# Kernel tuning notes

Measured on AMD Instinct MI355X. Metric: run time of the kernel, lower is better.

The kernel has to match this reference:

```python
import jax, jax.numpy as jnp
import numpy as np

D, K, H1, H2 = 768, 4, 512, 256
B = 16384

def layer_norm(x, g, b, eps=1e-5):
    mu = jnp.mean(x, axis=-1, keepdims=True)
    xc = x - mu
    var = jnp.mean(xc * xc, axis=-1, keepdims=True)
    return xc * jax.lax.rsqrt(var + eps) * g + b

def setup_inputs() -> dict:
    key = jax.random.key(0)
    ks = jax.random.split(key, 8)
    def lin(k, fan_in, fan_out):
        bound = 1.0 / np.sqrt(fan_in)
        kw, kb = jax.random.split(k)
        W = jax.random.uniform(kw, (fan_in, fan_out), jnp.float32, -bound, bound)
        b = jax.random.uniform(kb, (fan_out,), jnp.float32, -bound, bound)
        return W, b
    W1, b1 = lin(ks[0], D, H1)
    W2, b2 = lin(ks[1], H1, H2)
    Wd, bd = lin(ks[2], H2, K * D)
    Wa, ba = lin(ks[3], H2, D)
    return {
        "embeddings": jax.random.normal(ks[4], (B, D), jnp.float32),
        "W1": W1, "b1": b1, "g1": jnp.ones((H1,), jnp.float32), "be1": jnp.zeros((H1,), jnp.float32),
        "W2": W2, "b2": b2, "g2": jnp.ones((H2,), jnp.float32), "be2": jnp.zeros((H2,), jnp.float32),
        "Wd": Wd, "bd": bd, "Wa": Wa, "ba": ba,
    }

def _forward(embeddings, W1, b1, g1, be1, W2, b2, g2, be2, Wd, bd, Wa, ba):
    h = jax.nn.relu(layer_norm(embeddings @ W1 + b1, g1, be1))  # (B, H1)
    h = jax.nn.relu(layer_norm(h @ W2 + b2, g2, be2))           # (B, H2)
    W_flat = h @ Wd + bd                                         # (B, K*D)
    W = W_flat.reshape(-1, K, D)
    attn = jax.nn.softmax(h @ Wa + ba, axis=-1)                  # (B, D)
    W = W * attn[:, None, :]
    # sequential Gram-Schmidt over k (small fixed K, unrolled)
    ortho = []
    for i in range(K):
        v = W[:, i, :]
        for u in ortho:
            proj = jnp.sum(v * u, axis=-1, keepdims=True)
            v = v - proj * u
        norm = jnp.maximum(jnp.linalg.norm(v, axis=-1, keepdims=True), 1e-12)
        ortho.append(v / norm)
    W_ortho = jnp.stack(ortho, axis=1)  # (B, K, D)
    return W_ortho, attn

def reference(embeddings, W1, b1, g1, be1, W2, b2, g2, be2, Wd, bd, Wa, ba):
    return _forward(embeddings, W1, b1, g1, be1, W2, b2, g2, be2, Wd, bd, Wa, ba)
```

## Files before the change

### kernel.cpp

```cpp
#include <hip/hip_runtime.h>
#include <hip/hip_bf16.h>

#define BSZ 16384
#define DD  768
#define KK  4
#define NH1 512
#define NH2 256
#define ND  (KK * DD)

typedef __bf16 bf16x8 __attribute__((ext_vector_type(8)));
typedef float  f32x4  __attribute__((ext_vector_type(4)));

static __device__ __forceinline__ float bf2f(ushort u) {
    union { unsigned int i; float f; } v; v.i = (unsigned int)u << 16; return v.f;
}
static __device__ __forceinline__ ushort f2bf(float f) {
    return __bfloat16_as_ushort(__float2bfloat16(f));
}
static __device__ __forceinline__ void gload_lds16(const void* g, void* l) {
    __builtin_amdgcn_global_load_lds(
        (const __attribute__((address_space(1))) void*)g,
        (__attribute__((address_space(3))) void*)l, 16, 0, 0);
}

__global__ __launch_bounds__(256) void k_cvt_emb(
    const float* __restrict__ src, ushort* __restrict__ dst, int n8)
{
    const int stride = gridDim.x * 256;
    for (int i = blockIdx.x * 256 + threadIdx.x; i < n8; i += stride) {
        float4 a = *(const float4*)&src[(size_t)i * 8];
        float4 b = *(const float4*)&src[(size_t)i * 8 + 4];
        ushort u[8];
        u[0] = f2bf(a.x); u[1] = f2bf(a.y); u[2] = f2bf(a.z); u[3] = f2bf(a.w);
        u[4] = f2bf(b.x); u[5] = f2bf(b.y); u[6] = f2bf(b.z); u[7] = f2bf(b.w);
        *(int4*)&dst[(size_t)i * 8] = *(int4*)u;
    }
}

__global__ __launch_bounds__(256) void k_t_cvt(
    const float* __restrict__ src, ushort* __restrict__ dst, int R, int C)
{
    __shared__ float tile[32][33];
    const int rb0 = blockIdx.y * 32;
    const int cb0 = blockIdx.x * 32;
    const int t = threadIdx.x;
    const int r = t >> 5, c = t & 31;
    #pragma unroll
    for (int i = 0; i < 4; ++i)
        tile[r + i * 8][c] = src[(size_t)(rb0 + r + i * 8) * C + cb0 + c];
    __syncthreads();
    #pragma unroll
    for (int i = 0; i < 4; ++i)
        dst[(size_t)(cb0 + r + i * 8) * R + rb0 + c] = f2bf(tile[c][r + i * 8]);
}

__global__ __launch_bounds__(256) void k1_gemm(
    const ushort* __restrict__ embb, const ushort* __restrict__ W1t,
    const float* __restrict__ b1, ushort* __restrict__ h1raw)
{
    __shared__ ushort smem[2 * 128 * 64];
    ushort* Asm = smem;
    ushort* Bsm = smem + 128 * 64;

    const int t    = threadIdx.x;
    const int lane = t & 63;
    const int wid  = t >> 6;
    const int wm   = wid >> 1;
    const int wn   = wid & 1;
    const int l16  = lane & 15;
    const int sl0  = lane >> 4;
    const int g4   = (lane >> 4) * 4;

    const int srow = lane >> 3;
    const int ssl  = (lane & 7) ^ srow;

    const int rb = blockIdx.y * 128;
    const int cb = blockIdx.x * 128;

    f32x4 acc[4][4] = {};

    for (int ks = 0; ks < 12; ++ks) {
        const int k0 = ks * 64;
        __syncthreads();
        #pragma unroll
        for (int i = 0; i < 4; ++i) {
            const int stripe = wid * 4 + i;
            const int row    = stripe * 8 + srow;
            gload_lds16(&embb[(size_t)(rb + row) * DD + k0 + ssl * 8],
                        &Asm[stripe * 512]);
            gload_lds16(&W1t [(size_t)(cb + row) * DD + k0 + ssl * 8],
                        &Bsm[stripe * 512]);
        }
        __syncthreads();

        #pragma unroll
        for (int kk = 0; kk < 2; ++kk) {
            const int slot = kk * 4 + sl0;
            bf16x8 af[4], bfr[4];
            #pragma unroll
            for (int m = 0; m < 4; ++m) {
                const int R = wm * 64 + m * 16 + l16;
                af[m] = *(const bf16x8*)&Asm[R * 64 + (slot ^ (R & 7)) * 8];
            }
            #pragma unroll
            for (int n = 0; n < 4; ++n) {
                const int R = wn * 64 + n * 16 + l16;
                bfr[n] = *(const bf16x8*)&Bsm[R * 64 + (slot ^ (R & 7)) * 8];
            }
            #pragma unroll
            for (int m = 0; m < 4; ++m)
                #pragma unroll
                for (int n = 0; n < 4; ++n)
                    acc[m][n] = __builtin_amdgcn_mfma_f32_16x16x32_bf16(
                        af[m], bfr[n], acc[m][n], 0, 0, 0);
        }
    }

    float bv[4];
    #pragma unroll
    for (int n = 0; n < 4; ++n)
        bv[n] = b1[cb + wn * 64 + n * 16 + l16];

    __syncthreads();
    #pragma unroll
    for (int m = 0; m < 4; ++m)
        #pragma unroll
        for (int n = 0; n < 4; ++n)
            #pragma unroll
            for (int j = 0; j < 4; ++j)
                smem[(wm * 64 + m * 16 + g4 + j) * 128 + wn * 64 + n * 16 + l16] =
                    f2bf(acc[m][n][j] + bv[n]);
    __syncthreads();
    #pragma unroll
    for (int i = 0; i < 8; ++i) {
        int ch  = t + i * 256;
        int row = ch >> 4;
        int q   = ch & 15;
        *(int4*)&h1raw[(size_t)(rb + row) * NH1 + cb + q * 8] =
            *(const int4*)&smem[row * 128 + q * 8];
    }
}

__global__ __launch_bounds__(256) void k1_ln(
    ushort* h1, const float* __restrict__ g1, const float* __restrict__ be1)
{
    const int lane = threadIdx.x & 63;
    const int w    = threadIdx.x >> 6;
    const size_t row = (size_t)blockIdx.x * 4 + w;

    ushort* p = h1 + row * NH1 + lane * 8;
    ushort u[8];
    *(int4*)u = *(const int4*)p;
    float x[8];
    float s = 0.f, q = 0.f;
    #pragma unroll
    for (int j = 0; j < 8; ++j) {
        x[j] = bf2f(u[j]);
        s += x[j];
        q += x[j] * x[j];
    }
    #pragma unroll
    for (int off = 32; off; off >>= 1) {
        s += __shfl_xor(s, off);
        q += __shfl_xor(q, off);
    }
    const float mu  = s * (1.f / NH1);
    const float var = q * (1.f / NH1) - mu * mu;
    const float rs  = rsqrtf(var + 1e-5f);

    float gv[8], ev[8];
    *(float4*)&gv[0] = *(const float4*)&g1[lane * 8];
    *(float4*)&gv[4] = *(const float4*)&g1[lane * 8 + 4];
    *(float4*)&ev[0] = *(const float4*)&be1[lane * 8];
    *(float4*)&ev[4] = *(const float4*)&be1[lane * 8 + 4];
    #pragma unroll
    for (int j = 0; j < 8; ++j)
        u[j] = f2bf(fmaxf(fmaf((x[j] - mu) * rs, gv[j], ev[j]), 0.f));
    *(int4*)p = *(int4*)u;
}

__global__ __launch_bounds__(512) void k2_mfma(
    const ushort* __restrict__ h1, const ushort* __restrict__ W2t,
    const float* __restrict__ b2, const float* __restrict__ g2,
    const float* __restrict__ be2, ushort* __restrict__ h2)
{
    __shared__ ushort Asm[64 * 64];
    __shared__ ushort Bsm[256 * 64];
    __shared__ float red[8][64][2];
    __shared__ float stats[64][2];

    const int t    = threadIdx.x;
    const int lane = t & 63;
    const int wid  = t >> 6;
    const int wm   = wid >> 2;
    const int wn   = wid & 3;
    const int l16  = lane & 15;
    const int sl0  = lane >> 4;
    const int g4   = (lane >> 4) * 4;
    const int rb   = blockIdx.x * 64;

    const int srow = lane >> 3;
    const int ssl  = (lane & 7) ^ srow;

    f32x4 acc[2][4] = {};

    for (int ks = 0; ks < 8; ++ks) {
        const int k0 = ks * 64;
        __syncthreads();
        {
            const int row = wid * 8 + srow;
            gload_lds16(&h1[(size_t)(rb + row) * NH1 + k0 + ssl * 8],
                        &Asm[wid * 512]);
        }
        #pragma unroll
        for (int i = 0; i < 4; ++i) {
            const int stripe = wid * 4 + i;
            const int row    = stripe * 8 + srow;
            gload_lds16(&W2t[(size_t)row * NH1 + k0 + ssl * 8],
                        &Bsm[stripe * 512]);
        }
        __syncthreads();

        #pragma unroll
        for (int kk = 0; kk < 2; ++kk) {
            const int slot = kk * 4 + sl0;
            bf16x8 af[2], bfr[4];
            #pragma unroll
            for (int m = 0; m < 2; ++m) {
                const int R = wm * 32 + m * 16 + l16;
                af[m] = *(const bf16x8*)&Asm[R * 64 + (slot ^ (R & 7)) * 8];
            }
            #pragma unroll
            for (int n = 0; n < 4; ++n) {
                const int R = wn * 64 + n * 16 + l16;
                bfr[n] = *(const bf16x8*)&Bsm[R * 64 + (slot ^ (R & 7)) * 8];
            }
            #pragma unroll
            for (int m = 0; m < 2; ++m)
                #pragma unroll
                for (int n = 0; n < 4; ++n)
                    acc[m][n] = __builtin_amdgcn_mfma_f32_16x16x32_bf16(
                        af[m], bfr[n], acc[m][n], 0, 0, 0);
        }
    }

    float bv[4];
    #pragma unroll
    for (int n = 0; n < 4; ++n) bv[n] = b2[wn * 64 + n * 16 + l16];
    #pragma unroll
    for (int m = 0; m < 2; ++m)
        #pragma unroll
        for (int n = 0; n < 4; ++n)
            #pragma unroll
            for (int j = 0; j < 4; ++j) acc[m][n][j] += bv[n];

    #pragma unroll
    for (int m = 0; m < 2; ++m)
        #pragma unroll
        for (int j = 0; j < 4; ++j) {
            float p = 0.f, q = 0.f;
            #pragma unroll
            for (int n = 0; n < 4; ++n) {
                float v = acc[m][n][j];
                p += v; q += v * v;
            }
            #pragma unroll
            for (int off = 8; off; off >>= 1) {
                p += __shfl_xor(p, off);
                q += __shfl_xor(q, off);
            }
            if (l16 == 0) {
                red[wid][wm * 32 + m * 16 + g4 + j][0] = p;
                red[wid][wm * 32 + m * 16 + g4 + j][1] = q;
            }
        }
    __syncthreads();
    if (t < 64) {
        const int w0 = (t >> 5) * 4;
        float S = 0.f, S2 = 0.f;
        #pragma unroll
        for (int w = 0; w < 4; ++w) { S += red[w0 + w][t][0]; S2 += red[w0 + w][t][1]; }
        float mu  = S  * (1.f / NH2);
        float var = S2 * (1.f / NH2) - mu * mu;
        stats[t][0] = mu;
        stats[t][1] = rsqrtf(var + 1e-5f);
    }
    __syncthreads();

    float gv[4], ev[4];
    #pragma unroll
    for (int n = 0; n < 4; ++n) {
        int col = wn * 64 + n * 16 + l16;
        gv[n] = g2[col]; ev[n] = be2[col];
    }
    ushort* dst = h2 + (size_t)rb * NH2;
    #pragma unroll
    for (int m = 0; m < 2; ++m)
        #pragma unroll
        for (int j = 0; j < 4; ++j) {
            int row = wm * 32 + m * 16 + g4 + j;
            float mu = stats[row][0], rs = stats[row][1];
            #pragma unroll
            for (int n = 0; n < 4; ++n) {
                float val = fmaxf(fmaf((acc[m][n][j] - mu) * rs, gv[n], ev[n]), 0.f);
                dst[(size_t)row * NH2 + wn * 64 + n * 16 + l16] = f2bf(val);
            }
        }
}

__global__ __launch_bounds__(256) void k_gemm_wd_mfma(
    const ushort* __restrict__ h2, const ushort* __restrict__ Wdt,
    const float* __restrict__ bd, ushort* __restrict__ outw)
{
    __shared__ ushort smem[2 * 128 * 64];
    ushort* Asm = smem;
    ushort* Bsm = smem + 128 * 64;

    const int t    = threadIdx.x;
    const int lane = t & 63;
    const int wid  = t >> 6;
    const int wm   = wid >> 1;
    const int wn   = wid & 1;
    const int l16  = lane & 15;
    const int sl0  = lane >> 4;
    const int g4   = (lane >> 4) * 4;

    const int srow = lane >> 3;
    const int ssl  = (lane & 7) ^ srow;

    const int rb = blockIdx.y * 128;
    const int cb = blockIdx.x * 128;

    f32x4 acc[4][4] = {};

    for (int ks = 0; ks < 4; ++ks) {
        const int k0 = ks * 64;
        __syncthreads();
        #pragma unroll
        for (int i = 0; i < 4; ++i) {
            const int stripe = wid * 4 + i;
            const int row    = stripe * 8 + srow;
            gload_lds16(&h2 [(size_t)(rb + row) * NH2 + k0 + ssl * 8],
                        &Asm[stripe * 512]);
            gload_lds16(&Wdt[(size_t)(cb + row) * NH2 + k0 + ssl * 8],
                        &Bsm[stripe * 512]);
        }
        __syncthreads();

        #pragma unroll
        for (int kk = 0; kk < 2; ++kk) {
            const int slot = kk * 4 + sl0;
            bf16x8 af[4], bfr[4];
            #pragma unroll
            for (int m = 0; m < 4; ++m) {
                const int R = wm * 64 + m * 16 + l16;
                af[m] = *(const bf16x8*)&Asm[R * 64 + (slot ^ (R & 7)) * 8];
            }
            #pragma unroll
            for (int n = 0; n < 4; ++n) {
                const int R = wn * 64 + n * 16 + l16;
                bfr[n] = *(const bf16x8*)&Bsm[R * 64 + (slot ^ (R & 7)) * 8];
            }
            #pragma unroll
            for (int m = 0; m < 4; ++m)
                #pragma unroll
                for (int n = 0; n < 4; ++n)
                    acc[m][n] = __builtin_amdgcn_mfma_f32_16x16x32_bf16(
                        af[m], bfr[n], acc[m][n], 0, 0, 0);
        }
    }

    float bv[4];
    #pragma unroll
    for (int n = 0; n < 4; ++n)
        bv[n] = bd[cb + wn * 64 + n * 16 + l16];

    __syncthreads();
    #pragma unroll
    for (int m = 0; m < 4; ++m)
        #pragma unroll
        for (int n = 0; n < 4; ++n)
            #pragma unroll
            for (int j = 0; j < 4; ++j)
                smem[(wm * 64 + m * 16 + g4 + j) * 128 + wn * 64 + n * 16 + l16] =
                    f2bf(acc[m][n][j] + bv[n]);
    __syncthreads();
    #pragma unroll
    for (int i = 0; i < 8; ++i) {
        int ch  = t + i * 256;
        int row = ch >> 4;
        int q   = ch & 15;
        *(int4*)&outw[(size_t)(rb + row) * 6144 + 3072 + cb + q * 8] =
            *(const int4*)&smem[row * 128 + q * 8];
    }
}

__global__ __launch_bounds__(512) void k_attn_gs_mfma(
    const ushort* __restrict__ h2, const ushort* __restrict__ Wat,
    const float* __restrict__ ba, float* __restrict__ out)
{
    __shared__ ushort Asm[64 * 64];
    __shared__ ushort Bsm[768 * 64];
    __shared__ float red[8][64];
    __shared__ float stats[64];

    const int t    = threadIdx.x;
    const int lane = t & 63;
    const int wid  = t >> 6;
    const int wm   = wid >> 2;
    const int wn   = wid & 3;
    const int l16  = lane & 15;
    const int sl0  = lane >> 4;
    const int g4   = (lane >> 4) * 4;
    const int rb   = blockIdx.x * 64;

    const int srow = lane >> 3;
    const int ssl  = (lane & 7) ^ srow;

    float* attn = out + (size_t)BSZ * (KK * DD);

    f32x4 acc[2][12] = {};

    for (int ks = 0; ks < 4; ++ks) {
        const int k0 = ks * 64;
        __syncthreads();
        {
            const int row = wid * 8 + srow;
            gload_lds16(&h2[(size_t)(rb + row) * NH2 + k0 + ssl * 8],
                        &Asm[wid * 512]);
        }
        #pragma unroll
        for (int i = 0; i < 12; ++i) {
            const int stripe = wid * 12 + i;
            const int row    = stripe * 8 + srow;
            gload_lds16(&Wat[(size_t)row * NH2 + k0 + ssl * 8],
                        &Bsm[stripe * 512]);
        }
        __syncthreads();

        #pragma unroll
        for (int kk = 0; kk < 2; ++kk) {
            const int slot = kk * 4 + sl0;
            bf16x8 af[2], bfr[12];
            #pragma unroll
            for (int m = 0; m < 2; ++m) {
                const int R = wm * 32 + m * 16 + l16;
                af[m] = *(const bf16x8*)&Asm[R * 64 + (slot ^ (R & 7)) * 8];
            }
            #pragma unroll
            for (int n = 0; n < 12; ++n) {
                const int R = wn * 192 + n * 16 + l16;
                bfr[n] = *(const bf16x8*)&Bsm[R * 64 + (slot ^ (R & 7)) * 8];
            }
            #pragma unroll
            for (int m = 0; m < 2; ++m)
                #pragma unroll
                for (int n = 0; n < 12; ++n)
                    acc[m][n] = __builtin_amdgcn_mfma_f32_16x16x32_bf16(
                        af[m], bfr[n], acc[m][n], 0, 0, 0);
        }
    }

    float bb[12];
    #pragma unroll
    for (int n = 0; n < 12; ++n) bb[n] = ba[wn * 192 + n * 16 + l16];
    #pragma unroll
    for (int m = 0; m < 2; ++m)
        #pragma unroll
        for (int n = 0; n < 12; ++n)
            #pragma unroll
            for (int j = 0; j < 4; ++j) acc[m][n][j] += bb[n];

    #pragma unroll
    for (int m = 0; m < 2; ++m)
        #pragma unroll
        for (int j = 0; j < 4; ++j) {
            float p = acc[m][0][j];
            #pragma unroll
            for (int n = 1; n < 12; ++n) p = fmaxf(p, acc[m][n][j]);
            #pragma unroll
            for (int off = 8; off; off >>= 1) p = fmaxf(p, __shfl_xor(p, off));
            if (l16 == 0) red[wid][wm * 32 + m * 16 + g4 + j] = p;
        }
    __syncthreads();
    if (t < 64) {
        const int w0 = (t >> 5) * 4;
        stats[t] = fmaxf(fmaxf(red[w0][t], red[w0 + 1][t]),
                         fmaxf(red[w0 + 2][t], red[w0 + 3][t]));
    }
    __syncthreads();
    #pragma unroll
    for (int m = 0; m < 2; ++m)
        #pragma unroll
        for (int j = 0; j < 4; ++j) {
            float M = stats[wm * 32 + m * 16 + g4 + j];
            float s = 0.f;
            #pragma unroll
            for (int n = 0; n < 12; ++n) {
                acc[m][n][j] = __expf(acc[m][n][j] - M);
                s += acc[m][n][j];
            }
            #pragma unroll
            for (int off = 8; off; off >>= 1) s += __shfl_xor(s, off);
            if (l16 == 0) red[wid][wm * 32 + m * 16 + g4 + j] = s;
        }
    __syncthreads();
    if (t < 64) {
        const int w0 = (t >> 5) * 4;
        stats[t] = 1.f / (red[w0][t] + red[w0 + 1][t] + red[w0 + 2][t] + red[w0 + 3][t]);
    }
    __syncthreads();

    float* stage = (float*)Bsm;
    #pragma unroll
    for (int h = 0; h < 2; ++h) {
        if (wm == h) {
            #pragma unroll
            for (int m = 0; m < 2; ++m)
                #pragma unroll
                for (int j = 0; j < 4; ++j) {
                    const int r = m * 16 + g4 + j;
                    const float inv = stats[h * 32 + r];
                    #pragma unroll
                    for (int n = 0; n < 12; ++n)
                        stage[r * 768 + wn * 192 + n * 16 + l16] = acc[m][n][j] * inv;
                }
        }
        __syncthreads();
        #pragma unroll
        for (int i = 0; i < 12; ++i) {
            int ch  = t + i * 512;
            int row = ch / 192;
            int q   = ch - row * 192;
            *(float4*)&attn[(size_t)(rb + h * 32 + row) * DD + q * 4] =
                *(const float4*)&stage[row * 768 + q * 4];
        }
        for (int rr = 0; rr < 4; ++rr) {
            const int rl = wid * 4 + rr;
            const size_t row = (size_t)rb + h * 32 + rl;
            float a[12];
            #pragma unroll
            for (int k = 0; k < 3; ++k)
                *(float4*)&a[k * 4] =
                    *(const float4*)&stage[rl * 768 + lane * 4 + 256 * k];

            const ushort* wsrc = (const ushort*)out + row * 6144 + 3072;
            float* Wf = out + row * (KK * DD);
            float w[4][12];
            #pragma unroll
            for (int i = 0; i < 4; ++i) {
                #pragma unroll
                for (int k = 0; k < 3; ++k) {
                    ushort4 uv = *(const ushort4*)&wsrc[i * DD + lane * 4 + 256 * k];
                    w[i][k * 4 + 0] = bf2f(uv.x) * a[k * 4 + 0];
                    w[i][k * 4 + 1] = bf2f(uv.y) * a[k * 4 + 1];
                    w[i][k * 4 + 2] = bf2f(uv.z) * a[k * 4 + 2];
                    w[i][k * 4 + 3] = bf2f(uv.w) * a[k * 4 + 3];
                }
            }
            #pragma unroll
            for (int i = 0; i < 4; ++i) {
                #pragma unroll
                for (int p = 0; p < i; ++p) {
                    float s2 = 0.f;
                    #pragma unroll
                    for (int j = 0; j < 12; ++j) s2 = fmaf(w[i][j], w[p][j], s2);
                    #pragma unroll
                    for (int off = 32; off; off >>= 1) s2 += __shfl_xor(s2, off);
                    #pragma unroll
                    for (int j = 0; j < 12; ++j) w[i][j] = fmaf(-s2, w[p][j], w[i][j]);
                }
                float n2 = 0.f;
                #pragma unroll
                for (int j = 0; j < 12; ++j) n2 = fmaf(w[i][j], w[i][j], n2);
                #pragma unroll
                for (int off = 32; off; off >>= 1) n2 += __shfl_xor(n2, off);
                float invn = 1.f / fmaxf(sqrtf(n2), 1e-12f);
                #pragma unroll
                for (int j = 0; j < 12; ++j) w[i][j] *= invn;
            }
            #pragma unroll
            for (int i = 0; i < 4; ++i) {
                #pragma unroll
                for (int k = 0; k < 3; ++k) {
                    float4 wv;
                    wv.x = w[i][k * 4 + 0]; wv.y = w[i][k * 4 + 1];
                    wv.z = w[i][k * 4 + 2]; wv.w = w[i][k * 4 + 3];
                    *(float4*)&Wf[i * DD + lane * 4 + 256 * k] = wv;
                }
            }
        }
        __syncthreads();
    }
}

extern "C" void kernel_launch(void* const* d_in, const int* in_sizes, int n_in,
                              void* d_out, int out_size, void* d_ws, size_t ws_size,
                              hipStream_t stream)
{
    const float* emb = (const float*)d_in[0];
    const float* W1  = (const float*)d_in[1];
    const float* b1  = (const float*)d_in[2];
    const float* g1  = (const float*)d_in[3];
    const float* be1 = (const float*)d_in[4];
    const float* W2  = (const float*)d_in[5];
    const float* b2  = (const float*)d_in[6];
    const float* g2  = (const float*)d_in[7];
    const float* be2 = (const float*)d_in[8];
    const float* Wd  = (const float*)d_in[9];
    const float* bd  = (const float*)d_in[10];
    const float* Wa  = (const float*)d_in[11];
    const float* ba  = (const float*)d_in[12];

    float* out = (float*)d_out;
    ushort* h1   = (ushort*)d_ws;
    ushort* h2   = h1 + (size_t)BSZ * NH1;
    ushort* Wdt  = h2 + (size_t)BSZ * NH2;
    ushort* W1t  = Wdt + (size_t)ND * NH2;
    ushort* W2t  = W1t + (size_t)NH1 * DD;
    ushort* Wat  = W2t + (size_t)NH2 * NH1;
    ushort* embb = Wat + (size_t)DD * NH2;

    hipLaunchKernelGGL(k_cvt_emb, dim3(2048), dim3(256), 0, stream,
                       emb, embb, BSZ * DD / 8);
    hipLaunchKernelGGL(k_t_cvt, dim3(NH1 / 32, DD / 32), dim3(256), 0, stream,
                       W1, W1t, DD, NH1);
    hipLaunchKernelGGL(k_t_cvt, dim3(NH2 / 32, NH1 / 32), dim3(256), 0, stream,
                       W2, W2t, NH1, NH2);
    hipLaunchKernelGGL(k_t_cvt, dim3(ND / 32, NH2 / 32), dim3(256), 0, stream,
                       Wd, Wdt, NH2, ND);
    hipLaunchKernelGGL(k_t_cvt, dim3(DD / 32, NH2 / 32), dim3(256), 0, stream,
                       Wa, Wat, NH2, DD);
    hipLaunchKernelGGL(k1_gemm, dim3(NH1 / 128, BSZ / 128), dim3(256), 0, stream,
                       embb, W1t, b1, h1);
    hipLaunchKernelGGL(k1_ln, dim3(BSZ / 4), dim3(256), 0, stream,
                       h1, g1, be1);
    hipLaunchKernelGGL(k2_mfma, dim3(BSZ / 64), dim3(512), 0, stream,
                       h1, W2t, b2, g2, be2, h2);
    hipLaunchKernelGGL(k_gemm_wd_mfma, dim3(ND / 128, BSZ / 128), dim3(256), 0, stream,
                       h2, Wdt, bd, (ushort*)out);
    hipLaunchKernelGGL(k_attn_gs_mfma, dim3(BSZ / 64), dim3(512), 0, stream,
                       h2, Wat, ba, out);
}
```

Measured before the change: 181.5 us.

## Fuse LN1 into second GEMM and merge prep kernels into one launch

```diff
diff --git a/kernel.cpp b/kernel.cpp
--- a/kernel.cpp
+++ b/kernel.cpp
@@ -23,27 +23,41 @@
         (__attribute__((address_space(3))) void*)l, 16, 0, 0);
 }
 
-__global__ __launch_bounds__(256) void k_cvt_emb(
-    const float* __restrict__ src, ushort* __restrict__ dst, int n8)
-{
-    const int stride = gridDim.x * 256;
-    for (int i = blockIdx.x * 256 + threadIdx.x; i < n8; i += stride) {
-        float4 a = *(const float4*)&src[(size_t)i * 8];
-        float4 b = *(const float4*)&src[(size_t)i * 8 + 4];
-        ushort u[8];
-        u[0] = f2bf(a.x); u[1] = f2bf(a.y); u[2] = f2bf(a.z); u[3] = f2bf(a.w);
-        u[4] = f2bf(b.x); u[5] = f2bf(b.y); u[6] = f2bf(b.z); u[7] = f2bf(b.w);
-        *(int4*)&dst[(size_t)i * 8] = *(int4*)u;
-    }
-}
-
-__global__ __launch_bounds__(256) void k_t_cvt(
-    const float* __restrict__ src, ushort* __restrict__ dst, int R, int C)
+__global__ __launch_bounds__(256) void k_prep(
+    const float* __restrict__ emb, ushort* __restrict__ embb,
+    const float* __restrict__ W1, ushort* __restrict__ W1t,
+    const float* __restrict__ W2, ushort* __restrict__ W2t,
+    const float* __restrict__ Wd, ushort* __restrict__ Wdt,
+    const float* __restrict__ Wa, ushort* __restrict__ Wat)
 {
     __shared__ float tile[32][33];
-    const int rb0 = blockIdx.y * 32;
-    const int cb0 = blockIdx.x * 32;
+    const int bid = blockIdx.x;
     const int t = threadIdx.x;
+
+    if (bid < 2048) {
+        const int n8 = BSZ * DD / 8;
+        const int stride = 2048 * 256;
+        for (int i = bid * 256 + t; i < n8; i += stride) {
+            float4 a = *(const float4*)&emb[(size_t)i * 8];
+            float4 b = *(const float4*)&emb[(size_t)i * 8 + 4];
+            ushort u[8];
+            u[0] = f2bf(a.x); u[1] = f2bf(a.y); u[2] = f2bf(a.z); u[3] = f2bf(a.w);
+            u[4] = f2bf(b.x); u[5] = f2bf(b.y); u[6] = f2bf(b.z); u[7] = f2bf(b.w);
+            *(int4*)&embb[(size_t)i * 8] = *(int4*)u;
+        }
+        return;
+    }
+
+    const float* src; ushort* dst; int R, C, rb0, cb0;
+    if (bid < 2432)      { int l = bid - 2048; src = W1; dst = W1t; R = DD;  C = NH1;
+                           cb0 = (l & 15) * 32; rb0 = (l >> 4) * 32; }
+    else if (bid < 2560) { int l = bid - 2432; src = W2; dst = W2t; R = NH1; C = NH2;
+                           cb0 = (l & 7) * 32;  rb0 = (l >> 3) * 32; }
+    else if (bid < 3328) { int l = bid - 2560; src = Wd; dst = Wdt; R = NH2; C = ND;
+                           cb0 = (l % 96) * 32; rb0 = (l / 96) * 32; }
+    else                 { int l = bid - 3328; src = Wa; dst = Wat; R = NH2; C = DD;
+                           cb0 = (l % 24) * 32; rb0 = (l / 24) * 32; }
+
     const int r = t >> 5, c = t & 31;
     #pragma unroll
     for (int i = 0; i < 4; ++i)
@@ -141,116 +155,129 @@
     }
 }
 
-__global__ __launch_bounds__(256) void k1_ln(
-    ushort* h1, const float* __restrict__ g1, const float* __restrict__ be1)
-{
-    const int lane = threadIdx.x & 63;
-    const int w    = threadIdx.x >> 6;
-    const size_t row = (size_t)blockIdx.x * 4 + w;
-
-    ushort* p = h1 + row * NH1 + lane * 8;
-    ushort u[8];
-    *(int4*)u = *(const int4*)p;
-    float x[8];
-    float s = 0.f, q = 0.f;
-    #pragma unroll
-    for (int j = 0; j < 8; ++j) {
-        x[j] = bf2f(u[j]);
-        s += x[j];
-        q += x[j] * x[j];
-    }
-    #pragma unroll
-    for (int off = 32; off; off >>= 1) {
-        s += __shfl_xor(s, off);
-        q += __shfl_xor(q, off);
-    }
-    const float mu  = s * (1.f / NH1);
-    const float var = q * (1.f / NH1) - mu * mu;
-    const float rs  = rsqrtf(var + 1e-5f);
-
-    float gv[8], ev[8];
-    *(float4*)&gv[0] = *(const float4*)&g1[lane * 8];
-    *(float4*)&gv[4] = *(const float4*)&g1[lane * 8 + 4];
-    *(float4*)&ev[0] = *(const float4*)&be1[lane * 8];
-    *(float4*)&ev[4] = *(const float4*)&be1[lane * 8 + 4];
-    #pragma unroll
-    for (int j = 0; j < 8; ++j)
-        u[j] = f2bf(fmaxf(fmaf((x[j] - mu) * rs, gv[j], ev[j]), 0.f));
-    *(int4*)p = *(int4*)u;
-}
-
 __global__ __launch_bounds__(512) void k2_mfma(
-    const ushort* __restrict__ h1, const ushort* __restrict__ W2t,
+    const ushort* __restrict__ h1raw, const ushort* __restrict__ W2t,
+    const float* __restrict__ g1, const float* __restrict__ be1,
     const float* __restrict__ b2, const float* __restrict__ g2,
     const float* __restrict__ be2, ushort* __restrict__ h2)
 {
-    __shared__ ushort Asm[64 * 64];
+    __shared__ ushort Ah[8 * 2048];
     __shared__ ushort Bsm[256 * 64];
-    __shared__ float red[8][64][2];
-    __shared__ float stats[64][2];
+    __shared__ float red[8][32][2];
+    __shared__ float stats[32][2];
 
     const int t    = threadIdx.x;
     const int lane = t & 63;
     const int wid  = t >> 6;
-    const int wm   = wid >> 2;
-    const int wn   = wid & 3;
     const int l16  = lane & 15;
     const int sl0  = lane >> 4;
     const int g4   = (lane >> 4) * 4;
-    const int rb   = blockIdx.x * 64;
+    const int rb   = blockIdx.x * 32;
 
     const int srow = lane >> 3;
     const int ssl  = (lane & 7) ^ srow;
 
-    f32x4 acc[2][4] = {};
+    #pragma unroll
+    for (int i = 0; i < 4; ++i) {
+        const int s  = wid * 4 + i;
+        const int ks = s >> 2;
+        const int st = s & 3;
+        const int row = st * 8 + srow;
+        gload_lds16(&h1raw[(size_t)(rb + row) * NH1 + ks * 64 + ssl * 8],
+                    &Ah[ks * 2048 + st * 512]);
+    }
+    __syncthreads();
+
+    {
+        const int r  = t >> 4;
+        const int j  = t & 15;
+        const int ks = j >> 1;
+        const int hf = j & 1;
+        ushort u[4][8];
+        float s = 0.f, q2 = 0.f;
+        #pragma unroll
+        for (int qi = 0; qi < 4; ++qi) {
+            const int q = hf * 4 + qi;
+            *(int4*)u[qi] = *(const int4*)
+                &Ah[ks * 2048 + (r >> 3) * 512 + (r & 7) * 64 + ((q ^ (r & 7)) * 8)];
+            #pragma unroll
+            for (int e = 0; e < 8; ++e) {
+                float x = bf2f(u[qi][e]);
+                s += x; q2 += x * x;
+            }
+        }
+        #pragma unroll
+        for (int off = 8; off; off >>= 1) {
+            s  += __shfl_xor(s, off);
+            q2 += __shfl_xor(q2, off);
+        }
+        const float mu  = s * (1.f / NH1);
+        const float var = q2 * (1.f / NH1) - mu * mu;
+        const float rs  = rsqrtf(var + 1e-5f);
+        #pragma unroll
+        for (int qi = 0; qi < 4; ++qi) {
+            const int q = hf * 4 + qi;
+            const int col = ks * 64 + q * 8;
+            float gv[8], ev[8];
+            *(float4*)&gv[0] = *(const float4*)&g1[col];
+            *(float4*)&gv[4] = *(const float4*)&g1[col + 4];
+            *(float4*)&ev[0] = *(const float4*)&be1[col];
+            *(float4*)&ev[4] = *(const float4*)&be1[col + 4];
+            #pragma unroll
+            for (int e = 0; e < 8; ++e) {
+                float x = bf2f(u[qi][e]);
+                u[qi][e] = f2bf(fmaxf(fmaf((x - mu) * rs, gv[e], ev[e]), 0.f));
+            }
+            *(int4*)&Ah[ks * 2048 + (r >> 3) * 512 + (r & 7) * 64 + ((q ^ (r & 7)) * 8)]
+                = *(int4*)u[qi];
+        }
+    }
+
+    f32x4 acc[2][2] = {};
 
     for (int ks = 0; ks < 8; ++ks) {
         const int k0 = ks * 64;
         __syncthreads();
-        {
-            const int row = wid * 8 + srow;
-            gload_lds16(&h1[(size_t)(rb + row) * NH1 + k0 + ssl * 8],
-                        &Asm[wid * 512]);
-        }
         #pragma unroll
         for (int i = 0; i < 4; ++i) {
-            const int stripe = wid * 4 + i;
-            const int row    = stripe * 8 + srow;
+            const int s   = wid * 4 + i;
+            const int row = s * 8 + srow;
             gload_lds16(&W2t[(size_t)row * NH1 + k0 + ssl * 8],
-                        &Bsm[stripe * 512]);
+                        &Bsm[s * 512]);
         }
         __syncthreads();
 
         #pragma unroll
         for (int kk = 0; kk < 2; ++kk) {
             const int slot = kk * 4 + sl0;
-            bf16x8 af[2], bfr[4];
+            bf16x8 af[2], bfr[2];
             #pragma unroll
             for (int m = 0; m < 2; ++m) {
-                const int R = wm * 32 + m * 16 + l16;
-                af[m] = *(const bf16x8*)&Asm[R * 64 + (slot ^ (R & 7)) * 8];
-            }
-            #pragma unroll
-            for (int n = 0; n < 4; ++n) {
-                const int R = wn * 64 + n * 16 + l16;
+                const int R = m * 16 + l16;
+                af[m] = *(const bf16x8*)
+                    &Ah[ks * 2048 + R * 64 + (slot ^ (R & 7)) * 8];
+            }
+            #pragma unroll
+            for (int n = 0; n < 2; ++n) {
+                const int R = wid * 32 + n * 16 + l16;
                 bfr[n] = *(const bf16x8*)&Bsm[R * 64 + (slot ^ (R & 7)) * 8];
             }
             #pragma unroll
             for (int m = 0; m < 2; ++m)
                 #pragma unroll
-                for (int n = 0; n < 4; ++n)
+                for (int n = 0; n < 2; ++n)
                     acc[m][n] = __builtin_amdgcn_mfma_f32_16x16x32_bf16(
                         af[m], bfr[n], acc[m][n], 0, 0, 0);
         }
     }
 
-    float bv[4];
-    #pragma unroll
-    for (int n = 0; n < 4; ++n) bv[n] = b2[wn * 64 + n * 16 + l16];
+    float bv[2];
+    #pragma unroll
+    for (int n = 0; n < 2; ++n) bv[n] = b2[wid * 32 + n * 16 + l16];
     #pragma unroll
     for (int m = 0; m < 2; ++m)
         #pragma unroll
-        for (int n = 0; n < 4; ++n)
+        for (int n = 0; n < 2; ++n)
             #pragma unroll
             for (int j = 0; j < 4; ++j) acc[m][n][j] += bv[n];
 
@@ -260,7 +287,7 @@
         for (int j = 0; j < 4; ++j) {
             float p = 0.f, q = 0.f;
             #pragma unroll
-            for (int n = 0; n < 4; ++n) {
+            for (int n = 0; n < 2; ++n) {
                 float v = acc[m][n][j];
                 p += v; q += v * v;
             }
@@ -270,16 +297,15 @@
                 q += __shfl_xor(q, off);
             }
             if (l16 == 0) {
-                red[wid][wm * 32 + m * 16 + g4 + j][0] = p;
-                red[wid][wm * 32 + m * 16 + g4 + j][1] = q;
-            }
-        }
-    __syncthreads();
-    if (t < 64) {
-        const int w0 = (t >> 5) * 4;
+                red[wid][m * 16 + g4 + j][0] = p;
+                red[wid][m * 16 + g4 + j][1] = q;
+            }
+        }
+    __syncthreads();
+    if (t < 32) {
         float S = 0.f, S2 = 0.f;
         #pragma unroll
-        for (int w = 0; w < 4; ++w) { S += red[w0 + w][t][0]; S2 += red[w0 + w][t][1]; }
+        for (int w = 0; w < 8; ++w) { S += red[w][t][0]; S2 += red[w][t][1]; }
         float mu  = S  * (1.f / NH2);
         float var = S2 * (1.f / NH2) - mu * mu;
         stats[t][0] = mu;
@@ -287,10 +313,10 @@
     }
     __syncthreads();
 
-    float gv[4], ev[4];
-    #pragma unroll
-    for (int n = 0; n < 4; ++n) {
-        int col = wn * 64 + n * 16 + l16;
+    float gv[2], ev[2];
+    #pragma unroll
+    for (int n = 0; n < 2; ++n) {
+        int col = wid * 32 + n * 16 + l16;
         gv[n] = g2[col]; ev[n] = be2[col];
     }
     ushort* dst = h2 + (size_t)rb * NH2;
@@ -298,12 +324,12 @@
     for (int m = 0; m < 2; ++m)
         #pragma unroll
         for (int j = 0; j < 4; ++j) {
-            int row = wm * 32 + m * 16 + g4 + j;
+            int row = m * 16 + g4 + j;
             float mu = stats[row][0], rs = stats[row][1];
             #pragma unroll
-            for (int n = 0; n < 4; ++n) {
+            for (int n = 0; n < 2; ++n) {
                 float val = fmaxf(fmaf((acc[m][n][j] - mu) * rs, gv[n], ev[n]), 0.f);
-                dst[(size_t)row * NH2 + wn * 64 + n * 16 + l16] = f2bf(val);
+                dst[(size_t)row * NH2 + wid * 32 + n * 16 + l16] = f2bf(val);
             }
         }
 }
@@ -621,22 +647,12 @@
     ushort* Wat  = W2t + (size_t)NH2 * NH1;
     ushort* embb = Wat + (size_t)DD * NH2;
 
-    hipLaunchKernelGGL(k_cvt_emb, dim3(2048), dim3(256), 0, stream,
-                       emb, embb, BSZ * DD / 8);
-    hipLaunchKernelGGL(k_t_cvt, dim3(NH1 / 32, DD / 32), dim3(256), 0, stream,
-                       W1, W1t, DD, NH1);
-    hipLaunchKernelGGL(k_t_cvt, dim3(NH2 / 32, NH1 / 32), dim3(256), 0, stream,
-                       W2, W2t, NH1, NH2);
-    hipLaunchKernelGGL(k_t_cvt, dim3(ND / 32, NH2 / 32), dim3(256), 0, stream,
-                       Wd, Wdt, NH2, ND);
-    hipLaunchKernelGGL(k_t_cvt, dim3(DD / 32, NH2 / 32), dim3(256), 0, stream,
-                       Wa, Wat, NH2, DD);
+    hipLaunchKernelGGL(k_prep, dim3(3520), dim3(256), 0, stream,
+                       emb, embb, W1, W1t, W2, W2t, Wd, Wdt, Wa, Wat);
     hipLaunchKernelGGL(k1_gemm, dim3(NH1 / 128, BSZ / 128), dim3(256), 0, stream,
                        embb, W1t, b1, h1);
-    hipLaunchKernelGGL(k1_ln, dim3(BSZ / 4), dim3(256), 0, stream,
-                       h1, g1, be1);
-    hipLaunchKernelGGL(k2_mfma, dim3(BSZ / 64), dim3(512), 0, stream,
-                       h1, W2t, b2, g2, be2, h2);
+    hipLaunchKernelGGL(k2_mfma, dim3(BSZ / 32), dim3(512), 0, stream,
+                       h1, W2t, g1, be1, b2, g2, be2, h2);
     hipLaunchKernelGGL(k_gemm_wd_mfma, dim3(ND / 128, BSZ / 128), dim3(256), 0, stream,
                        h2, Wdt, bd, (ushort*)out);
     hipLaunchKernelGGL(k_attn_gs_mfma, dim3(BSZ / 64), dim3(512), 0, stream,
```

Result: faster. 174.2 us (median of 2 runs) (-4.0%).
